# Optimization experiments

Hardware: AMD Instinct MI355X
Metric: run time of the kernel (lower is better)

The kernel has to match this reference:

```python
import jax, jax.numpy as jnp
import numpy as np

NUM_LAYERS = 9
HIDDEN = 3


def _param_indices(hidden, num_layers):
    # Mirrors DistributionFreeModel.calculate_parameter_indices
    offset = 3 + (num_layers - 2) * (hidden + 2)
    idx = [((0 * hidden, 1 * hidden), (1 * hidden, 2 * hidden), (2 * hidden, 3 * hidden))]
    for o in range(3, offset, hidden + 2):
        idx.append((
            (o * hidden, (o + hidden) * hidden),
            ((o + hidden) * hidden, (o + hidden + 1) * hidden),
            ((o + hidden + 1) * hidden, (o + hidden + 2) * hidden),
        ))
    idx.append(((offset * hidden, (offset + 1) * hidden),
                ((offset + 1) * hidden, (offset + 1) * hidden + 1),
                None))
    return idx


def _cdf(inputs, parameters, hidden=HIDDEN, num_layers=NUM_LAYERS):
    # inputs: [B, F]; parameters: [F, P]
    out = inputs[..., None]  # [B, F, 1]
    for li, (wi, bi, si) in enumerate(_param_indices(hidden, num_layers)):
        w = parameters[..., wi[0]:wi[1]]
        b = parameters[..., bi[0]:bi[1]]
        if li == 0:
            w = w.reshape(w.shape[:-1] + (hidden, 1))
        elif li == num_layers - 1:
            w = w.reshape(w.shape[:-1] + (1, hidden))
        else:
            w = w.reshape(w.shape[:-1] + (hidden, hidden))
        w = jax.nn.softplus(w)
        # per-feature tiny matmul, broadcast over batch: [B,F,f] x [F,d,f] -> [B,F,d]
        out = jnp.einsum('...f,...df->...d', out, w) + b
        if si is not None:
            s = jnp.tanh(parameters[..., si[0]:si[1]])
            out = out + s * jnp.tanh(out)
    return jax.nn.sigmoid(out)[..., 0]  # squeeze last dim -> [B, F]


def setup_inputs() -> dict:
    key = jax.random.key(0)
    k1, k2 = jax.random.split(key)
    B, F = 32768, 512
    P = (NUM_LAYERS - 2) * HIDDEN ** 2 + 2 * NUM_LAYERS * HIDDEN + 1  # 118
    inputs = jax.random.normal(k1, (B, F), dtype=jnp.float32)
    parameters = jax.random.normal(k2, (F, P), dtype=jnp.float32)
    return {"inputs": inputs, "parameters": parameters}


def reference(inputs, parameters):
    return _cdf(inputs, parameters)
```

## Files before the change

### kernel.cpp

```cpp
#include <hip/hip_runtime.h>
#include <math.h>

#define NF 512
#define NP 118
#define NPPAD 126
#define FT 32
#define ROWS 8
#define BLOCK_ROWS 64
#define TBL_N 2048
#define WS_NEED ((size_t)(NPPAD * NF + 2 * TBL_N) * sizeof(float))

typedef float v2f __attribute__((ext_vector_type(2)));

__device__ __forceinline__ v2f f_PP(v2f a, v2f b, v2f c) {
    v2f d; asm("v_pk_fma_f32 %0, %1, %2, %3" : "=v"(d) : "v"(a), "v"(b), "v"(c)); return d;
}
__device__ __forceinline__ v2f f_LP(v2f a, v2f b, v2f c) {
    v2f d; asm("v_pk_fma_f32 %0, %1, %2, %3 op_sel_hi:[1,0,1]" : "=v"(d) : "v"(a), "v"(b), "v"(c)); return d;
}
__device__ __forceinline__ v2f f_HP(v2f a, v2f b, v2f c) {
    v2f d; asm("v_pk_fma_f32 %0, %1, %2, %3 op_sel:[0,1,0] op_sel_hi:[1,1,1]" : "=v"(d) : "v"(a), "v"(b), "v"(c)); return d;
}
__device__ __forceinline__ v2f f_LH(v2f a, v2f b, v2f c) {
    v2f d; asm("v_pk_fma_f32 %0, %1, %2, %3 op_sel:[0,0,1] op_sel_hi:[1,0,1]" : "=v"(d) : "v"(a), "v"(b), "v"(c)); return d;
}
__device__ __forceinline__ v2f f_HL(v2f a, v2f b, v2f c) {
    v2f d; asm("v_pk_fma_f32 %0, %1, %2, %3 op_sel:[0,1,0] op_sel_hi:[1,1,0]" : "=v"(d) : "v"(a), "v"(b), "v"(c)); return d;
}

__device__ __forceinline__ float fast_rcp(float x) { return __builtin_amdgcn_rcpf(x); }
__device__ __forceinline__ float exp2_fast(float x) {
#if __has_builtin(__builtin_amdgcn_exp2f)
    return __builtin_amdgcn_exp2f(x);
#else
    return __expf(x * 0.6931471805599453f);
#endif
}

__device__ __forceinline__ float tanh_exp1(float x) {
    float e = exp2_fast(x * 2.8853900817779268f);
    return fmaf(-2.0f, fast_rcp(e + 1.0f), 1.0f);
}
__device__ __forceinline__ v2f tanh_exp_pair(v2f a) {
    v2f t; t.x = tanh_exp1(a.x); t.y = tanh_exp1(a.y); return t;
}
__device__ __forceinline__ float sigmoid1(float x) {
    return fast_rcp(1.0f + exp2_fast(x * -1.4426950408889634f));
}

__device__ __forceinline__ v2f tanh_lut_pair(v2f a, const v2f* __restrict__ tbl,
                                             v2f K128, v2f KIdx) {
    v2f xi = f_PP(a, K128, KIdx);
    unsigned i0 = (unsigned)__builtin_amdgcn_fmed3f(xi.x, 0.0f, (float)(TBL_N - 1));
    unsigned i1 = (unsigned)__builtin_amdgcn_fmed3f(xi.y, 0.0f, (float)(TBL_N - 1));
    v2f g0 = tbl[i0];
    v2f g1 = tbl[i1];
    v2f t;
    t.x = fmaf(a.x, g0.x, g0.y);
    t.y = fmaf(a.y, g1.x, g1.y);
    return t;
}

__device__ __forceinline__ float transform_one(float v, int j) {
    int cls;
    if (j < 3) cls = 0;
    else if (j < 6) cls = 1;
    else if (j < 9) cls = 2;
    else if (j < 114) { int k = (j - 9) % 15; cls = (k < 9) ? 0 : ((k < 12) ? 1 : 2); }
    else if (j < 117) cls = 0;
    else cls = 1;
    if (cls == 0) return fmaxf(v, 0.0f) + log1pf(expf(-fabsf(v)));
    if (cls == 2) return tanhf(v);
    return v;
}

__device__ __forceinline__ bool map_padded(int jp, int* j) {
    if (jp < 9) { *j = jp; return true; }
    if (jp == 9) return false;
    if (jp < 122) {
        int k = (jp - 10) & 15, li = (jp - 10) >> 4;
        if (k == 15) return false;
        *j = 9 + 15 * li + k;
        return true;
    }
    *j = 114 + (jp - 122);
    return true;
}

__device__ __forceinline__ float transform_padded(const float* __restrict__ prow, int jp) {
    int j;
    if (!map_padded(jp, &j)) return 0.0f;
    return transform_one(prow[j], j);
}

__device__ __forceinline__ void tbl_entry(int b, float* s, float* c) {
    float xl = (float)b * (1.0f / 128.0f) - (1024.5f / 128.0f);
    float xr = xl + (1.0f / 128.0f);
    float t0 = tanhf(xl), t1 = tanhf(xr);
    float sl = (t1 - t0) * 128.0f;
    *s = sl;
    *c = fmaf(-sl, xl, t0);
}

__global__ void xform_kernel(const float* __restrict__ p, float* __restrict__ t) {
    int idx = blockIdx.x * 256 + threadIdx.x;
    if (idx < NPPAD * NF) {
        int jp = idx / NF, f = idx - jp * NF;
        t[idx] = transform_padded(p + f * NP, jp);
    } else if (idx < NPPAD * NF + TBL_N) {
        int bin = idx - NPPAD * NF;
        float s, c;
        tbl_entry(bin, &s, &c);
        t[NPPAD * NF + 2 * bin]     = s;
        t[NPPAD * NF + 2 * bin + 1] = c;
    }
}

template <bool FUSE_XFORM>
__global__ __launch_bounds__(256)
void cdf_kernel(const float* __restrict__ x, const float* __restrict__ prm,
                float* __restrict__ out) {
    __shared__ float ldsp[NPPAD * FT];
    __shared__ v2f   tblv[TBL_N];
    const int tid = threadIdx.x;
    const int fi  = tid & (FT - 1);
    const int rg  = tid >> 5;
    const int f0  = blockIdx.x * FT;
    const int b0  = blockIdx.y * BLOCK_ROWS + rg * ROWS;
    const int f   = f0 + fi;

    if constexpr (FUSE_XFORM) {
        for (int idx = tid; idx < NPPAD * FT; idx += 256) {
            int jp = idx >> 5, fl = idx & (FT - 1);
            ldsp[(jp >> 1) * (2 * FT) + fl * 2 + (jp & 1)] =
                transform_padded(prm + (f0 + fl) * NP, jp);
        }
        float* tf = (float*)tblv;
        for (int bin = tid; bin < TBL_N; bin += 256) {
            float s, c; tbl_entry(bin, &s, &c);
            tf[2 * bin] = s; tf[2 * bin + 1] = c;
        }
    } else {
        for (int idx = tid; idx < NPPAD * FT; idx += 256) {
            int jp = idx >> 5, fl = idx & (FT - 1);
            ldsp[(jp >> 1) * (2 * FT) + fl * 2 + (jp & 1)] = prm[jp * NF + f0 + fl];
        }
        float* tf = (float*)tblv;
        const float* tw = prm + NPPAD * NF;
        for (int idx = tid; idx < 2 * TBL_N; idx += 256)
            tf[idx] = tw[idx];
    }

    v2f xin[4];
#pragma unroll
    for (int r = 0; r < 4; ++r) {
        xin[r].x = x[(b0 + 2 * r)     * NF + f];
        xin[r].y = x[(b0 + 2 * r + 1) * NF + f];
    }

    __syncthreads();

    const v2f K128 = {128.0f, 128.0f};
    const v2f KIdx = {1024.5f, 1024.5f};

    const float* Pp = ldsp + fi * 2;
#define PRMV(JP) (*reinterpret_cast<const v2f*>(Pp + (JP) * FT))

    v2f h0[4], h1[4], h2[4];
    {
        v2f q0 = PRMV(0), q1 = PRMV(2), q2 = PRMV(4), q3 = PRMV(6), q4 = PRMV(8);
#pragma unroll
        for (int r = 0; r < 4; ++r) {
            v2f a0 = f_LH(xin[r], q0, q1);
            v2f a1 = f_HL(xin[r], q0, q2);
            v2f a2 = f_LH(xin[r], q1, q2);
            v2f T0 = tanh_lut_pair(a0, tblv, K128, KIdx);
            v2f T1 = tanh_lut_pair(a1, tblv, K128, KIdx);
            v2f T2 = tanh_exp_pair(a2);
            h0[r] = f_LP(T0, q3, a0);
            h1[r] = f_HP(T1, q3, a1);
            h2[r] = f_LP(T2, q4, a2);
        }
    }
#pragma unroll
    for (int li = 1; li < 8; ++li) {
        const int bp = 10 + 16 * (li - 1);
        v2f q0 = PRMV(bp + 0), q1 = PRMV(bp + 2), q2 = PRMV(bp + 4), q3 = PRMV(bp + 6);
        v2f q4 = PRMV(bp + 8), q5 = PRMV(bp + 10), q6 = PRMV(bp + 12), q7 = PRMV(bp + 14);
#pragma unroll
        for (int r = 0; r < 4; ++r) {
            v2f t0 = f_LH(h0[r], q0, q4);
            t0     = f_HP(h1[r], q0, t0);
            v2f a0 = f_LP(h2[r], q1, t0);
            v2f t1 = f_HL(h0[r], q1, q5);
            t1     = f_LP(h1[r], q2, t1);
            v2f a1 = f_HP(h2[r], q2, t1);
            v2f t2 = f_LH(h0[r], q3, q5);
            t2     = f_HP(h1[r], q3, t2);
            v2f a2 = f_LP(h2[r], q4, t2);
            v2f T0 = tanh_lut_pair(a0, tblv, K128, KIdx);
            v2f T1 = tanh_lut_pair(a1, tblv, K128, KIdx);
            v2f T2 = tanh_exp_pair(a2);
            h0[r] = f_LP(T0, q6, a0);
            h1[r] = f_HP(T1, q6, a1);
            h2[r] = f_LP(T2, q7, a2);
        }
    }
    {
        v2f q8 = PRMV(122), q9 = PRMV(124);
#pragma unroll
        for (int r = 0; r < 4; ++r) {
            v2f a = f_LH(h0[r], q8, q9);
            a     = f_HP(h1[r], q8, a);
            a     = f_LP(h2[r], q9, a);
            out[(b0 + 2 * r)     * NF + f] = sigmoid1(a.x);
            out[(b0 + 2 * r + 1) * NF + f] = sigmoid1(a.y);
        }
    }
#undef PRMV
}

extern "C" void kernel_launch(void* const* d_in, const int* in_sizes, int n_in,
                              void* d_out, int out_size, void* d_ws, size_t ws_size,
                              hipStream_t stream) {
    const float* x = (const float*)d_in[0];
    const float* p = (const float*)d_in[1];
    float* out = (float*)d_out;

    const int B = in_sizes[0] / NF;
    dim3 grid(NF / FT, B / BLOCK_ROWS);
    dim3 block(256);

    if (ws_size >= WS_NEED) {
        float* t = (float*)d_ws;
        int total = NPPAD * NF + TBL_N;
        xform_kernel<<<(total + 255) / 256, 256, 0, stream>>>(p, t);
        cdf_kernel<false><<<grid, block, 0, stream>>>(x, t, out);
    } else {
        cdf_kernel<true><<<grid, block, 0, stream>>>(x, p, out);
    }
}
```

Baseline: 111.2 us.

## Pack two adjacent features per lane instead of two batch rows

Each lane now packs two neighbouring features into the v2f instead of two batch rows of one feature. The per-feature parameters load straight as v2f pairs with plain packed FMAs, with no op_sel broadcasts. Global loads and stores become 8-byte vector accesses. The tile changes to 16 features by 128 rows with 4 rows per thread. This halves the parameter LDS footprint but makes each block reload the 16KB tanh table for a narrower feature slice, which may cost more LDS traffic per block.

Measured after the change: 103.6 us, median of 2. 1.07x faster.

```diff
diff --git a/kernel.cpp b/kernel.cpp
--- a/kernel.cpp
+++ b/kernel.cpp
@@ -4,9 +4,10 @@
 #define NF 512
 #define NP 118
 #define NPPAD 126
-#define FT 32
-#define ROWS 8
-#define BLOCK_ROWS 64
+#define FT 16
+#define NPF 8
+#define ROWS 4
+#define BLOCK_ROWS 128
 #define TBL_N 2048
 #define WS_NEED ((size_t)(NPPAD * NF + 2 * TBL_N) * sizeof(float))
 
@@ -14,18 +15,6 @@
 
 __device__ __forceinline__ v2f f_PP(v2f a, v2f b, v2f c) {
     v2f d; asm("v_pk_fma_f32 %0, %1, %2, %3" : "=v"(d) : "v"(a), "v"(b), "v"(c)); return d;
-}
-__device__ __forceinline__ v2f f_LP(v2f a, v2f b, v2f c) {
-    v2f d; asm("v_pk_fma_f32 %0, %1, %2, %3 op_sel_hi:[1,0,1]" : "=v"(d) : "v"(a), "v"(b), "v"(c)); return d;
-}
-__device__ __forceinline__ v2f f_HP(v2f a, v2f b, v2f c) {
-    v2f d; asm("v_pk_fma_f32 %0, %1, %2, %3 op_sel:[0,1,0] op_sel_hi:[1,1,1]" : "=v"(d) : "v"(a), "v"(b), "v"(c)); return d;
-}
-__device__ __forceinline__ v2f f_LH(v2f a, v2f b, v2f c) {
-    v2f d; asm("v_pk_fma_f32 %0, %1, %2, %3 op_sel:[0,0,1] op_sel_hi:[1,0,1]" : "=v"(d) : "v"(a), "v"(b), "v"(c)); return d;
-}
-__device__ __forceinline__ v2f f_HL(v2f a, v2f b, v2f c) {
-    v2f d; asm("v_pk_fma_f32 %0, %1, %2, %3 op_sel:[0,1,0] op_sel_hi:[1,1,0]" : "=v"(d) : "v"(a), "v"(b), "v"(c)); return d;
 }
 
 __device__ __forceinline__ float fast_rcp(float x) { return __builtin_amdgcn_rcpf(x); }
@@ -120,20 +109,19 @@
 __global__ __launch_bounds__(256)
 void cdf_kernel(const float* __restrict__ x, const float* __restrict__ prm,
                 float* __restrict__ out) {
-    __shared__ float ldsp[NPPAD * FT];
-    __shared__ v2f   tblv[TBL_N];
+    __shared__ __attribute__((aligned(16))) float ldsp[NPPAD * FT];
+    __shared__ v2f tblv[TBL_N];
     const int tid = threadIdx.x;
-    const int fi  = tid & (FT - 1);
-    const int rg  = tid >> 5;
+    const int pf  = tid & (NPF - 1);
+    const int rg  = tid >> 3;
     const int f0  = blockIdx.x * FT;
     const int b0  = blockIdx.y * BLOCK_ROWS + rg * ROWS;
-    const int f   = f0 + fi;
+    const int fe  = f0 + 2 * pf;
 
     if constexpr (FUSE_XFORM) {
         for (int idx = tid; idx < NPPAD * FT; idx += 256) {
-            int jp = idx >> 5, fl = idx & (FT - 1);
-            ldsp[(jp >> 1) * (2 * FT) + fl * 2 + (jp & 1)] =
-                transform_padded(prm + (f0 + fl) * NP, jp);
+            int jp = idx >> 4, fl = idx & (FT - 1);
+            ldsp[idx] = transform_padded(prm + (f0 + fl) * NP, jp);
         }
         float* tf = (float*)tblv;
         for (int bin = tid; bin < TBL_N; bin += 256) {
@@ -142,8 +130,8 @@
         }
     } else {
         for (int idx = tid; idx < NPPAD * FT; idx += 256) {
-            int jp = idx >> 5, fl = idx & (FT - 1);
-            ldsp[(jp >> 1) * (2 * FT) + fl * 2 + (jp & 1)] = prm[jp * NF + f0 + fl];
+            int jp = idx >> 4, fl = idx & (FT - 1);
+            ldsp[idx] = prm[jp * NF + f0 + fl];
         }
         float* tf = (float*)tblv;
         const float* tw = prm + NPPAD * NF;
@@ -151,70 +139,67 @@
             tf[idx] = tw[idx];
     }
 
-    v2f xin[4];
-#pragma unroll
-    for (int r = 0; r < 4; ++r) {
-        xin[r].x = x[(b0 + 2 * r)     * NF + f];
-        xin[r].y = x[(b0 + 2 * r + 1) * NF + f];
-    }
+    v2f xin[ROWS];
+#pragma unroll
+    for (int r = 0; r < ROWS; ++r)
+        xin[r] = *reinterpret_cast<const v2f*>(&x[(b0 + r) * NF + fe]);
 
     __syncthreads();
 
     const v2f K128 = {128.0f, 128.0f};
     const v2f KIdx = {1024.5f, 1024.5f};
 
-    const float* Pp = ldsp + fi * 2;
+    const float* Pp = ldsp + 2 * pf;
 #define PRMV(JP) (*reinterpret_cast<const v2f*>(Pp + (JP) * FT))
 
-    v2f h0[4], h1[4], h2[4];
+    v2f h0[ROWS], h1[ROWS], h2[ROWS];
     {
-        v2f q0 = PRMV(0), q1 = PRMV(2), q2 = PRMV(4), q3 = PRMV(6), q4 = PRMV(8);
-#pragma unroll
-        for (int r = 0; r < 4; ++r) {
-            v2f a0 = f_LH(xin[r], q0, q1);
-            v2f a1 = f_HL(xin[r], q0, q2);
-            v2f a2 = f_LH(xin[r], q1, q2);
+        v2f W0 = PRMV(0), W1 = PRMV(1), W2 = PRMV(2);
+        v2f C0 = PRMV(3), C1 = PRMV(4), C2 = PRMV(5);
+        v2f S0 = PRMV(6), S1 = PRMV(7), S2 = PRMV(8);
+#pragma unroll
+        for (int r = 0; r < ROWS; ++r) {
+            v2f a0 = f_PP(xin[r], W0, C0);
+            v2f a1 = f_PP(xin[r], W1, C1);
+            v2f a2 = f_PP(xin[r], W2, C2);
             v2f T0 = tanh_lut_pair(a0, tblv, K128, KIdx);
             v2f T1 = tanh_lut_pair(a1, tblv, K128, KIdx);
             v2f T2 = tanh_exp_pair(a2);
-            h0[r] = f_LP(T0, q3, a0);
-            h1[r] = f_HP(T1, q3, a1);
-            h2[r] = f_LP(T2, q4, a2);
+            h0[r] = f_PP(S0, T0, a0);
+            h1[r] = f_PP(S1, T1, a1);
+            h2[r] = f_PP(S2, T2, a2);
         }
     }
 #pragma unroll
     for (int li = 1; li < 8; ++li) {
         const int bp = 10 + 16 * (li - 1);
-        v2f q0 = PRMV(bp + 0), q1 = PRMV(bp + 2), q2 = PRMV(bp + 4), q3 = PRMV(bp + 6);
-        v2f q4 = PRMV(bp + 8), q5 = PRMV(bp + 10), q6 = PRMV(bp + 12), q7 = PRMV(bp + 14);
-#pragma unroll
-        for (int r = 0; r < 4; ++r) {
-            v2f t0 = f_LH(h0[r], q0, q4);
-            t0     = f_HP(h1[r], q0, t0);
-            v2f a0 = f_LP(h2[r], q1, t0);
-            v2f t1 = f_HL(h0[r], q1, q5);
-            t1     = f_LP(h1[r], q2, t1);
-            v2f a1 = f_HP(h2[r], q2, t1);
-            v2f t2 = f_LH(h0[r], q3, q5);
-            t2     = f_HP(h1[r], q3, t2);
-            v2f a2 = f_LP(h2[r], q4, t2);
+        v2f W00 = PRMV(bp + 0), W01 = PRMV(bp + 1), W02 = PRMV(bp + 2);
+        v2f W10 = PRMV(bp + 3), W11 = PRMV(bp + 4), W12 = PRMV(bp + 5);
+        v2f W20 = PRMV(bp + 6), W21 = PRMV(bp + 7), W22 = PRMV(bp + 8);
+        v2f C0  = PRMV(bp + 9), C1  = PRMV(bp + 10), C2 = PRMV(bp + 11);
+        v2f S0  = PRMV(bp + 12), S1 = PRMV(bp + 13), S2 = PRMV(bp + 14);
+#pragma unroll
+        for (int r = 0; r < ROWS; ++r) {
+            v2f a0 = f_PP(h0[r], W00, f_PP(h1[r], W01, f_PP(h2[r], W02, C0)));
+            v2f a1 = f_PP(h0[r], W10, f_PP(h1[r], W11, f_PP(h2[r], W12, C1)));
+            v2f a2 = f_PP(h0[r], W20, f_PP(h1[r], W21, f_PP(h2[r], W22, C2)));
             v2f T0 = tanh_lut_pair(a0, tblv, K128, KIdx);
             v2f T1 = tanh_lut_pair(a1, tblv, K128, KIdx);
             v2f T2 = tanh_exp_pair(a2);
-            h0[r] = f_LP(T0, q6, a0);
-            h1[r] = f_HP(T1, q6, a1);
-            h2[r] = f_LP(T2, q7, a2);
+            h0[r] = f_PP(S0, T0, a0);
+            h1[r] = f_PP(S1, T1, a1);
+            h2[r] = f_PP(S2, T2, a2);
         }
     }
     {
-        v2f q8 = PRMV(122), q9 = PRMV(124);
-#pragma unroll
-        for (int r = 0; r < 4; ++r) {
-            v2f a = f_LH(h0[r], q8, q9);
-            a     = f_HP(h1[r], q8, a);
-            a     = f_LP(h2[r], q9, a);
-            out[(b0 + 2 * r)     * NF + f] = sigmoid1(a.x);
-            out[(b0 + 2 * r + 1) * NF + f] = sigmoid1(a.y);
+        v2f W0 = PRMV(122), W1 = PRMV(123), W2 = PRMV(124), CB = PRMV(125);
+#pragma unroll
+        for (int r = 0; r < ROWS; ++r) {
+            v2f a = f_PP(h0[r], W0, f_PP(h1[r], W1, f_PP(h2[r], W2, CB)));
+            v2f o;
+            o.x = sigmoid1(a.x);
+            o.y = sigmoid1(a.y);
+            *reinterpret_cast<v2f*>(&out[(b0 + r) * NF + fe]) = o;
         }
     }
 #undef PRMV
```
